# Performance work log

Hardware: AMD Instinct MI355X
Metric: run time of the kernel (lower is better)

## Reference

```python
import jax, jax.numpy as jnp
import numpy as np

B, S, D_MODEL, H = 4, 2048, 1024, 16
D_K = D_MODEL // H


def setup_inputs() -> dict:
    key = jax.random.key(0)
    kx, kq, kk, kv, ko = jax.random.split(key, 5)
    scale = 1.0 / np.sqrt(D_MODEL)
    return {
        "x": jax.random.normal(kx, (B, S, D_MODEL), dtype=jnp.float32),
        "W_q": jax.random.normal(kq, (D_MODEL, D_MODEL), dtype=jnp.float32) * scale,
        "W_k": jax.random.normal(kk, (D_MODEL, D_MODEL), dtype=jnp.float32) * scale,
        "W_v": jax.random.normal(kv, (D_MODEL, D_MODEL), dtype=jnp.float32) * scale,
        "W_out": jax.random.normal(ko, (D_MODEL, D_MODEL), dtype=jnp.float32) * scale,
    }


def reference(x, W_q, W_k, W_v, W_out):
    # nn.Linear(bias=False): y = x @ W.T; weights stored as (out, in).
    Bx, Sx, D = x.shape
    q = (x @ W_q.T).reshape(Bx, Sx, H, D_K).transpose(0, 2, 1, 3)  # (B,H,S,d_k)
    k = (x @ W_k.T).reshape(Bx, Sx, H, D_K).transpose(0, 2, 1, 3)
    v = (x @ W_v.T).reshape(Bx, Sx, H, D_K).transpose(0, 2, 1, 3)
    scores = jnp.einsum("bhsd,bhtd->bhst", q, k) / jnp.sqrt(jnp.float32(D_K))
    attn = jax.nn.softmax(scores, axis=-1)
    out = jnp.einsum("bhst,bhtd->bhsd", attn, v)  # (B,H,S,d_k)
    out = out.transpose(0, 2, 1, 3).reshape(Bx, Sx, D)  # combine heads
    return out @ W_out.T
```

## Files before the change

### kernel.cpp

```cpp
#include <hip/hip_runtime.h>

#define BATCH 4
#define SEQ 2048
#define DM 1024
#define NH 16
#define DK 64

typedef unsigned short u16;
typedef unsigned int u32;
typedef __attribute__((ext_vector_type(8))) short bfrag;
typedef __attribute__((ext_vector_type(4))) short bfrag4;
typedef __attribute__((ext_vector_type(4))) float ffrag;

__device__ inline u16 f2bf(float f) {
  union { float f; u32 u; } v; v.f = f;
  u32 u = v.u;
  return (u16)((u + 0x7FFFu + ((u >> 16) & 1u)) >> 16);
}
__device__ inline float bf2f(u16 u) {
  union { u32 u; float f; } v; v.u = ((u32)u) << 16;
  return v.f;
}
__device__ inline ffrag MFMA(bfrag a, bfrag b, ffrag c) {
  return __builtin_amdgcn_mfma_f32_16x16x32_bf16(a, b, c, 0, 0, 0);
}
#if defined(__has_builtin)
#if __has_builtin(__builtin_amdgcn_mfma_f32_16x16x16bf16_1k)
#define HAVE_MFMA16 1
#endif
#endif
#if HAVE_MFMA16
__device__ inline ffrag MFMA16(bfrag4 a, bfrag4 b, ffrag c) {
  return __builtin_amdgcn_mfma_f32_16x16x16bf16_1k(a, b, c, 0, 0, 0);
}
#else
__device__ inline ffrag MFMA16(bfrag4 a, bfrag4 b, ffrag c) { return c; }
#endif

__device__ __forceinline__ void g2l16(const u16* g, u16* l) {
  __builtin_amdgcn_global_load_lds(
      (const __attribute__((address_space(1))) u16*)g,
      (__attribute__((address_space(3))) u16*)l, 16, 0, 0);
}

__global__ __launch_bounds__(256) void cvt_all(
    const float* __restrict__ x,
    const float* __restrict__ a, const float* __restrict__ b,
    const float* __restrict__ c, const float* __restrict__ d,
    u16* __restrict__ ox,
    u16* __restrict__ oa, u16* __restrict__ ob,
    u16* __restrict__ oc, u16* __restrict__ od) {
  int blk = blockIdx.x;
  const float* in;
  u16* out;
  int i;
  if (blk < 8192) {
    in = x; out = ox; i = blk * 256 + threadIdx.x;
  } else {
    int wb = blk - 8192;
    int which = wb >> 10;
    in = which == 0 ? a : which == 1 ? b : which == 2 ? c : d;
    out = which == 0 ? oa : which == 1 ? ob : which == 2 ? oc : od;
    i = (wb & 1023) * 256 + threadIdx.x;
  }
  float4 v = ((const float4*)in)[i];
  union { u16 u[4]; uint2 dd; } o;
  o.u[0] = f2bf(v.x); o.u[1] = f2bf(v.y); o.u[2] = f2bf(v.z); o.u[3] = f2bf(v.w);
  ((uint2*)out)[i] = o.dd;
}

__global__ __launch_bounds__(256) void gemm_qkv(
    const u16* __restrict__ xb,
    const u16* __restrict__ Wq, const u16* __restrict__ Wk,
    const u16* __restrict__ Wv,
    u16* __restrict__ Qb, u16* __restrict__ Ksw, u16* __restrict__ Vsw) {
  const int z = blockIdx.z;
  const u16* Bm = z == 0 ? Wq : z == 1 ? Wk : Wv;

  const int K = DM;
  const int bm = blockIdx.y * 128, bn = blockIdx.x * 128;
  __shared__ __align__(16) u16 As[128 * 32];
  __shared__ __align__(16) u16 Bs[128 * 32];
  const int tid = threadIdx.x;
  const int lane = tid & 63;
  const int w = tid >> 6;
  const int wr = w >> 1, wc = w & 1;
  const int l15 = lane & 15, quad = lane >> 4;
  const int srow = tid >> 2, scol = (tid & 3) * 8;

  ffrag acc[4][4] = {};

  for (int k0 = 0; k0 < K; k0 += 32) {
    __syncthreads();
    g2l16(&xb[(size_t)(bm + srow) * K + k0 + scol], &As[tid * 8]);
    g2l16(&xb[(size_t)(bm + 64 + srow) * K + k0 + scol], &As[(tid + 256) * 8]);
    g2l16(&Bm[(size_t)(bn + srow) * K + k0 + scol], &Bs[tid * 8]);
    g2l16(&Bm[(size_t)(bn + 64 + srow) * K + k0 + scol], &Bs[(tid + 256) * 8]);
    __syncthreads();
    bfrag af[4], bf[4];
    if (z < 2) {
#pragma unroll
      for (int i = 0; i < 4; i++)
        af[i] = *(const bfrag*)(&As[(wr * 64 + i * 16 + l15) * 32 + quad * 8]);
#pragma unroll
      for (int j = 0; j < 4; j++)
        bf[j] = *(const bfrag*)(&Bs[(wc * 64 + j * 16 + l15) * 32 + quad * 8]);
    } else {
#pragma unroll
      for (int i = 0; i < 4; i++)
        af[i] = *(const bfrag*)(&Bs[(wr * 64 + i * 16 + l15) * 32 + quad * 8]);
#pragma unroll
      for (int j = 0; j < 4; j++)
        bf[j] = *(const bfrag*)(&As[(wc * 64 + j * 16 + l15) * 32 + quad * 8]);
    }
#pragma unroll
    for (int i = 0; i < 4; i++)
#pragma unroll
      for (int j = 0; j < 4; j++)
        acc[i][j] = MFMA(af[i], bf[j], acc[i][j]);
  }

  if (z == 0) {
#pragma unroll
    for (int i = 0; i < 4; i++)
#pragma unroll
      for (int j = 0; j < 4; j++)
#pragma unroll
        for (int r = 0; r < 4; r++) {
          int m = bm + wr * 64 + i * 16 + quad * 4 + r;
          int n = bn + wc * 64 + j * 16 + l15;
          int b = m >> 11, s = m & 2047;
          int h = n >> 6, d = n & 63;
          Qb[(((size_t)(b * NH + h)) * SEQ + s) * DK + d] = f2bf(acc[i][j][r]);
        }
  } else if (z == 1) {
#pragma unroll
    for (int i = 0; i < 4; i++)
#pragma unroll
      for (int j = 0; j < 4; j++)
#pragma unroll
        for (int r = 0; r < 4; r++) {
          int m = bm + wr * 64 + i * 16 + quad * 4 + r;
          int n = bn + wc * 64 + j * 16 + l15;
          int b = m >> 11, s = m & 2047;
          int h = n >> 6, d = n & 63;
          size_t hb = (size_t)(b * NH + h) * (SEQ * DK);
          size_t off = hb + (size_t)(s >> 6) * 4096 +
              ((((s >> 4) & 3) * 2 + (d >> 5)) * 64 +
               ((d >> 3) & 3) * 16 + (s & 15)) * 8 + (d & 7);
          Ksw[off] = f2bf(acc[i][j][r]);
        }
  } else {
#pragma unroll
    for (int i = 0; i < 4; i++)
#pragma unroll
      for (int j = 0; j < 4; j++)
#pragma unroll
        for (int r = 0; r < 4; r++) {
          int n = bn + wr * 64 + i * 16 + quad * 4 + r;
          int m = bm + wc * 64 + j * 16 + l15;
          int b = m >> 11, s = m & 2047;
          int h = n >> 6, d = n & 63;
          size_t hb = (size_t)(b * NH + h) * (SEQ * DK);
          size_t off = hb + (size_t)(s >> 6) * 4096 +
              ((((d >> 4) * 4 + ((s >> 4) & 3)) * 64 +
                ((s >> 2) & 3) * 16 + (d & 15)) * 4 + (s & 3));
          Vsw[off] = f2bf(acc[i][j][r]);
        }
  }
}

__global__ __launch_bounds__(256) void gemm_out(
    const u16* __restrict__ Ab, const u16* __restrict__ Wo, float* __restrict__ C) {
  const int K = DM, N = DM;
  const int bm = blockIdx.y * 128, bn = blockIdx.x * 128;
  __shared__ __align__(16) u16 As[128 * 32];
  __shared__ __align__(16) u16 Bs[128 * 32];
  const int tid = threadIdx.x;
  const int lane = tid & 63;
  const int w = tid >> 6;
  const int wr = w >> 1, wc = w & 1;
  const int l15 = lane & 15, quad = lane >> 4;
  const int srow = tid >> 2, scol = (tid & 3) * 8;

  ffrag acc[4][4] = {};

  for (int k0 = 0; k0 < K; k0 += 32) {
    __syncthreads();
    g2l16(&Ab[(size_t)(bm + srow) * K + k0 + scol], &As[tid * 8]);
    g2l16(&Ab[(size_t)(bm + 64 + srow) * K + k0 + scol], &As[(tid + 256) * 8]);
    g2l16(&Wo[(size_t)(bn + srow) * K + k0 + scol], &Bs[tid * 8]);
    g2l16(&Wo[(size_t)(bn + 64 + srow) * K + k0 + scol], &Bs[(tid + 256) * 8]);
    __syncthreads();
    bfrag af[4], bf[4];
#pragma unroll
    for (int i = 0; i < 4; i++)
      af[i] = *(const bfrag*)(&As[(wr * 64 + i * 16 + l15) * 32 + quad * 8]);
#pragma unroll
    for (int j = 0; j < 4; j++)
      bf[j] = *(const bfrag*)(&Bs[(wc * 64 + j * 16 + l15) * 32 + quad * 8]);
#pragma unroll
    for (int i = 0; i < 4; i++)
#pragma unroll
      for (int j = 0; j < 4; j++)
        acc[i][j] = MFMA(af[i], bf[j], acc[i][j]);
  }

#pragma unroll
  for (int i = 0; i < 4; i++)
#pragma unroll
    for (int j = 0; j < 4; j++)
#pragma unroll
      for (int r = 0; r < 4; r++) {
        int m = bm + wr * 64 + i * 16 + quad * 4 + r;
        int n = bn + wc * 64 + j * 16 + l15;
        C[(size_t)m * N + n] = acc[i][j][r];
      }
}

__global__ __launch_bounds__(256) void attn(
    const u16* __restrict__ Qb, const u16* __restrict__ Ksw,
    const u16* __restrict__ Vsw, u16* __restrict__ Ab) {
  const int bh = blockIdx.y;
  const int b = bh >> 4, h = bh & 15;
  const int qbase = blockIdx.x * 128;
  const int tid = threadIdx.x;
  const int w = tid >> 6, lane = tid & 63;
  const int l15 = lane & 15, quad = lane >> 4;

  __shared__ __align__(16) u16 Kt[2][4096];
  __shared__ __align__(16) u16 Vt[2][4096];

  const size_t hbase = (size_t)bh * SEQ * DK;

  const float qscale = 0.125f * 1.4426950408889634f;
  bfrag q[2][2];
#pragma unroll
  for (int i = 0; i < 2; i++)
#pragma unroll
    for (int kk = 0; kk < 2; kk++) {
      bfrag t = *(const bfrag*)(&Qb[hbase +
          (size_t)(qbase + w * 32 + i * 16 + l15) * DK + kk * 32 + quad * 8]);
#pragma unroll
      for (int e = 0; e < 8; e++)
        q[i][kk][e] = (short)f2bf(bf2f((u16)t[e]) * qscale);
    }

  ffrag O[4][2] = {};
  float lsum[2] = {0.f, 0.f};

  {
    const u16* ks = &Ksw[hbase];
    const u16* vs = &Vsw[hbase];
    g2l16(&ks[tid * 8], &Kt[0][tid * 8]);
    g2l16(&ks[2048 + tid * 8], &Kt[0][2048 + tid * 8]);
    g2l16(&vs[tid * 8], &Vt[0][tid * 8]);
    g2l16(&vs[2048 + tid * 8], &Vt[0][2048 + tid * 8]);
  }

  for (int t = 0; t < SEQ / 64; t++) {
    const int buf = t & 1;
    __syncthreads();
    if (t + 1 < SEQ / 64) {
      const u16* ks = &Ksw[hbase + (size_t)(t + 1) * 4096];
      const u16* vs = &Vsw[hbase + (size_t)(t + 1) * 4096];
      g2l16(&ks[tid * 8], &Kt[buf ^ 1][tid * 8]);
      g2l16(&ks[2048 + tid * 8], &Kt[buf ^ 1][2048 + tid * 8]);
      g2l16(&vs[tid * 8], &Vt[buf ^ 1][tid * 8]);
      g2l16(&vs[2048 + tid * 8], &Vt[buf ^ 1][2048 + tid * 8]);
    }

    __builtin_amdgcn_s_setprio(1);
    bfrag4 pb[4][2];
#pragma unroll
    for (int j = 0; j < 4; j++) {
      bfrag k0f = *(const bfrag*)(&Kt[buf][((j * 2 + 0) * 64 + lane) * 8]);
      bfrag k1f = *(const bfrag*)(&Kt[buf][((j * 2 + 1) * 64 + lane) * 8]);
#pragma unroll
      for (int i = 0; i < 2; i++) {
        ffrag z = {};
        z = MFMA(k0f, q[i][0], z);
        z = MFMA(k1f, q[i][1], z);
        u32 u[4]; float ts = 0.f;
#pragma unroll
        for (int r = 0; r < 4; r++) {
          float p = __builtin_amdgcn_exp2f(z[r]);
          u[r] = __float_as_uint(p);
          ts += __uint_as_float(u[r] & 0xffff0000u);
        }
        lsum[i] += ts;
        union { u32 d[2]; bfrag4 v; } pk;
        pk.d[0] = (u[1] & 0xffff0000u) | (u[0] >> 16);
        pk.d[1] = (u[3] & 0xffff0000u) | (u[2] >> 16);
        pb[j][i] = pk.v;
      }
    }

#pragma unroll
    for (int j = 0; j < 4; j++)
#pragma unroll
      for (int db = 0; db < 4; db++) {
        bfrag4 vf = *(const bfrag4*)(&Vt[buf][((db * 4 + j) * 64 + lane) * 4]);
        O[db][0] = MFMA16(vf, pb[j][0], O[db][0]);
        O[db][1] = MFMA16(vf, pb[j][1], O[db][1]);
      }
    __builtin_amdgcn_s_setprio(0);
  }

  float rl[2];
#pragma unroll
  for (int i = 0; i < 2; i++) {
    float s = lsum[i];
    s += __shfl_xor(s, 16);
    s += __shfl_xor(s, 32);
    rl[i] = 1.0f / s;
  }

  const size_t obase = ((size_t)b * SEQ) * DM + (size_t)h * DK;
#pragma unroll
  for (int db = 0; db < 4; db++)
#pragma unroll
    for (int i = 0; i < 2; i++) {
      int s = qbase + w * 32 + i * 16 + l15;
      union { u16 u[4]; uint2 d; } o;
#pragma unroll
      for (int r = 0; r < 4; r++) o.u[r] = f2bf(O[db][i][r] * rl[i]);
      *(uint2*)(&Ab[obase + (size_t)s * DM + db * 16 + quad * 4]) = o.d;
    }
}

extern "C" void kernel_launch(void* const* d_in, const int* in_sizes, int n_in,
                              void* d_out, int out_size, void* d_ws, size_t ws_size,
                              hipStream_t stream) {
  const float* x  = (const float*)d_in[0];
  const float* Wq = (const float*)d_in[1];
  const float* Wk = (const float*)d_in[2];
  const float* Wv = (const float*)d_in[3];
  const float* Wo = (const float*)d_in[4];
  float* out = (float*)d_out;

  char* ws = (char*)d_ws;
  u16* xb  = (u16*)(ws + 0);
  u16* Wqb = (u16*)(ws + 16777216);
  u16* Wkb = (u16*)(ws + 18874368);
  u16* Wvb = (u16*)(ws + 20971520);
  u16* Wob = (u16*)(ws + 23068672);
  u16* Qb  = (u16*)(ws + 25165824);
  u16* Ksw = (u16*)(ws + 41943040);
  u16* Vsw = (u16*)(ws + 58720256);
  u16* Ab  = (u16*)(ws + 75497472);
  const size_t NEED = 92274688;
  if (ws_size < NEED) return;

  cvt_all<<<12288, 256, 0, stream>>>(x, Wq, Wk, Wv, Wo, xb, Wqb, Wkb, Wvb, Wob);

  dim3 gqkv(DM / 128, (BATCH * SEQ) / 128, 3);
  gemm_qkv<<<gqkv, 256, 0, stream>>>(xb, Wqb, Wkb, Wvb, Qb, Ksw, Vsw);

  dim3 gat(SEQ / 128, BATCH * NH);
  attn<<<gat, 256, 0, stream>>>(Qb, Ksw, Vsw, Ab);

  dim3 gout(DM / 128, (BATCH * SEQ) / 128);
  gemm_out<<<gout, 256, 0, stream>>>(Ab, Wob, out);
}
```

Baseline: 292.4 us.

## Widen GEMM K-tile with XOR-swizzled LDS, sum softmax via MFMA, reorder attn grid

Both projection GEMMs now stage a K-depth of 64 per iteration instead of 32, halving the number of barrier pairs, and store tiles in LDS with an XOR swizzle on 16-byte chunks to avoid bank conflicts. In attention, the per-lane scalar row-sum plus cross-lane shuffles is replaced by an extra MFMA against a vector of ones that accumulates the softmax denominator. The attention grid is transposed so consecutive blocks cover different heads for the same query tile. The trade-off is twice the LDS per GEMM block, which may reduce occupancy, and one extra MFMA per P tile in the attention loop.

Measured after the change: 298.8 us. 1.02x slower.

```diff
diff --git a/kernel.cpp b/kernel.cpp
--- a/kernel.cpp
+++ b/kernel.cpp
@@ -79,45 +79,54 @@
 
   const int K = DM;
   const int bm = blockIdx.y * 128, bn = blockIdx.x * 128;
-  __shared__ __align__(16) u16 As[128 * 32];
-  __shared__ __align__(16) u16 Bs[128 * 32];
+  __shared__ __align__(16) u16 As[128 * 64];
+  __shared__ __align__(16) u16 Bs[128 * 64];
   const int tid = threadIdx.x;
   const int lane = tid & 63;
   const int w = tid >> 6;
   const int wr = w >> 1, wc = w & 1;
   const int l15 = lane & 15, quad = lane >> 4;
-  const int srow = tid >> 2, scol = (tid & 3) * 8;
+  const int srow = tid >> 3;
+  const int scol = (((tid & 7) ^ (srow & 7)) * 8);
 
   ffrag acc[4][4] = {};
 
-  for (int k0 = 0; k0 < K; k0 += 32) {
-    __syncthreads();
-    g2l16(&xb[(size_t)(bm + srow) * K + k0 + scol], &As[tid * 8]);
-    g2l16(&xb[(size_t)(bm + 64 + srow) * K + k0 + scol], &As[(tid + 256) * 8]);
-    g2l16(&Bm[(size_t)(bn + srow) * K + k0 + scol], &Bs[tid * 8]);
-    g2l16(&Bm[(size_t)(bn + 64 + srow) * K + k0 + scol], &Bs[(tid + 256) * 8]);
-    __syncthreads();
-    bfrag af[4], bf[4];
-    if (z < 2) {
+  for (int k0 = 0; k0 < K; k0 += 64) {
+    __syncthreads();
+#pragma unroll
+    for (int c = 0; c < 4; c++) {
+      g2l16(&xb[(size_t)(bm + c * 32 + srow) * K + k0 + scol], &As[c * 2048 + tid * 8]);
+      g2l16(&Bm[(size_t)(bn + c * 32 + srow) * K + k0 + scol], &Bs[c * 2048 + tid * 8]);
+    }
+    __syncthreads();
+#pragma unroll
+    for (int kk = 0; kk < 2; kk++) {
+      bfrag af[4], bf[4];
+      if (z < 2) {
+#pragma unroll
+        for (int i = 0; i < 4; i++)
+          af[i] = *(const bfrag*)(&As[(wr * 64 + i * 16 + l15) * 64 +
+                                      ((kk * 4 + quad) ^ (l15 & 7)) * 8]);
+#pragma unroll
+        for (int j = 0; j < 4; j++)
+          bf[j] = *(const bfrag*)(&Bs[(wc * 64 + j * 16 + l15) * 64 +
+                                      ((kk * 4 + quad) ^ (l15 & 7)) * 8]);
+      } else {
+#pragma unroll
+        for (int i = 0; i < 4; i++)
+          af[i] = *(const bfrag*)(&Bs[(wr * 64 + i * 16 + l15) * 64 +
+                                      ((kk * 4 + quad) ^ (l15 & 7)) * 8]);
+#pragma unroll
+        for (int j = 0; j < 4; j++)
+          bf[j] = *(const bfrag*)(&As[(wc * 64 + j * 16 + l15) * 64 +
+                                      ((kk * 4 + quad) ^ (l15 & 7)) * 8]);
+      }
 #pragma unroll
       for (int i = 0; i < 4; i++)
-        af[i] = *(const bfrag*)(&As[(wr * 64 + i * 16 + l15) * 32 + quad * 8]);
-#pragma unroll
-      for (int j = 0; j < 4; j++)
-        bf[j] = *(const bfrag*)(&Bs[(wc * 64 + j * 16 + l15) * 32 + quad * 8]);
-    } else {
-#pragma unroll
-      for (int i = 0; i < 4; i++)
-        af[i] = *(const bfrag*)(&Bs[(wr * 64 + i * 16 + l15) * 32 + quad * 8]);
-#pragma unroll
-      for (int j = 0; j < 4; j++)
-        bf[j] = *(const bfrag*)(&As[(wc * 64 + j * 16 + l15) * 32 + quad * 8]);
-    }
-#pragma unroll
-    for (int i = 0; i < 4; i++)
-#pragma unroll
-      for (int j = 0; j < 4; j++)
-        acc[i][j] = MFMA(af[i], bf[j], acc[i][j]);
+#pragma unroll
+        for (int j = 0; j < 4; j++)
+          acc[i][j] = MFMA(af[i], bf[j], acc[i][j]);
+    }
   }
 
   if (z == 0) {
@@ -174,36 +183,43 @@
     const u16* __restrict__ Ab, const u16* __restrict__ Wo, float* __restrict__ C) {
   const int K = DM, N = DM;
   const int bm = blockIdx.y * 128, bn = blockIdx.x * 128;
-  __shared__ __align__(16) u16 As[128 * 32];
-  __shared__ __align__(16) u16 Bs[128 * 32];
+  __shared__ __align__(16) u16 As[128 * 64];
+  __shared__ __align__(16) u16 Bs[128 * 64];
   const int tid = threadIdx.x;
   const int lane = tid & 63;
   const int w = tid >> 6;
   const int wr = w >> 1, wc = w & 1;
   const int l15 = lane & 15, quad = lane >> 4;
-  const int srow = tid >> 2, scol = (tid & 3) * 8;
+  const int srow = tid >> 3;
+  const int scol = (((tid & 7) ^ (srow & 7)) * 8);
 
   ffrag acc[4][4] = {};
 
-  for (int k0 = 0; k0 < K; k0 += 32) {
-    __syncthreads();
-    g2l16(&Ab[(size_t)(bm + srow) * K + k0 + scol], &As[tid * 8]);
-    g2l16(&Ab[(size_t)(bm + 64 + srow) * K + k0 + scol], &As[(tid + 256) * 8]);
-    g2l16(&Wo[(size_t)(bn + srow) * K + k0 + scol], &Bs[tid * 8]);
-    g2l16(&Wo[(size_t)(bn + 64 + srow) * K + k0 + scol], &Bs[(tid + 256) * 8]);
-    __syncthreads();
-    bfrag af[4], bf[4];
-#pragma unroll
-    for (int i = 0; i < 4; i++)
-      af[i] = *(const bfrag*)(&As[(wr * 64 + i * 16 + l15) * 32 + quad * 8]);
-#pragma unroll
-    for (int j = 0; j < 4; j++)
-      bf[j] = *(const bfrag*)(&Bs[(wc * 64 + j * 16 + l15) * 32 + quad * 8]);
-#pragma unroll
-    for (int i = 0; i < 4; i++)
+  for (int k0 = 0; k0 < K; k0 += 64) {
+    __syncthreads();
+#pragma unroll
+    for (int c = 0; c < 4; c++) {
+      g2l16(&Ab[(size_t)(bm + c * 32 + srow) * K + k0 + scol], &As[c * 2048 + tid * 8]);
+      g2l16(&Wo[(size_t)(bn + c * 32 + srow) * K + k0 + scol], &Bs[c * 2048 + tid * 8]);
+    }
+    __syncthreads();
+#pragma unroll
+    for (int kk = 0; kk < 2; kk++) {
+      bfrag af[4], bf[4];
+#pragma unroll
+      for (int i = 0; i < 4; i++)
+        af[i] = *(const bfrag*)(&As[(wr * 64 + i * 16 + l15) * 64 +
+                                    ((kk * 4 + quad) ^ (l15 & 7)) * 8]);
 #pragma unroll
       for (int j = 0; j < 4; j++)
-        acc[i][j] = MFMA(af[i], bf[j], acc[i][j]);
+        bf[j] = *(const bfrag*)(&Bs[(wc * 64 + j * 16 + l15) * 64 +
+                                    ((kk * 4 + quad) ^ (l15 & 7)) * 8]);
+#pragma unroll
+      for (int i = 0; i < 4; i++)
+#pragma unroll
+        for (int j = 0; j < 4; j++)
+          acc[i][j] = MFMA(af[i], bf[j], acc[i][j]);
+    }
   }
 
 #pragma unroll
@@ -221,9 +237,9 @@
 __global__ __launch_bounds__(256) void attn(
     const u16* __restrict__ Qb, const u16* __restrict__ Ksw,
     const u16* __restrict__ Vsw, u16* __restrict__ Ab) {
-  const int bh = blockIdx.y;
+  const int bh = blockIdx.x;
   const int b = bh >> 4, h = bh & 15;
-  const int qbase = blockIdx.x * 128;
+  const int qbase = blockIdx.y * 128;
   const int tid = threadIdx.x;
   const int w = tid >> 6, lane = tid & 63;
   const int l15 = lane & 15, quad = lane >> 4;
@@ -246,8 +262,10 @@
         q[i][kk][e] = (short)f2bf(bf2f((u16)t[e]) * qscale);
     }
 
+  const bfrag4 ones = {(short)0x3F80, (short)0x3F80, (short)0x3F80, (short)0x3F80};
+
   ffrag O[4][2] = {};
-  float lsum[2] = {0.f, 0.f};
+  ffrag Ls[2] = {};
 
   {
     const u16* ks = &Ksw[hbase];
@@ -281,18 +299,15 @@
         ffrag z = {};
         z = MFMA(k0f, q[i][0], z);
         z = MFMA(k1f, q[i][1], z);
-        u32 u[4]; float ts = 0.f;
-#pragma unroll
-        for (int r = 0; r < 4; r++) {
-          float p = __builtin_amdgcn_exp2f(z[r]);
-          u[r] = __float_as_uint(p);
-          ts += __uint_as_float(u[r] & 0xffff0000u);
-        }
-        lsum[i] += ts;
+        u32 u0 = __float_as_uint(__builtin_amdgcn_exp2f(z[0]));
+        u32 u1 = __float_as_uint(__builtin_amdgcn_exp2f(z[1]));
+        u32 u2 = __float_as_uint(__builtin_amdgcn_exp2f(z[2]));
+        u32 u3 = __float_as_uint(__builtin_amdgcn_exp2f(z[3]));
         union { u32 d[2]; bfrag4 v; } pk;
-        pk.d[0] = (u[1] & 0xffff0000u) | (u[0] >> 16);
-        pk.d[1] = (u[3] & 0xffff0000u) | (u[2] >> 16);
+        pk.d[0] = (u1 & 0xffff0000u) | (u0 >> 16);
+        pk.d[1] = (u3 & 0xffff0000u) | (u2 >> 16);
         pb[j][i] = pk.v;
+        Ls[i] = MFMA16(ones, pb[j][i], Ls[i]);
       }
     }
 
@@ -307,14 +322,7 @@
     __builtin_amdgcn_s_setprio(0);
   }
 
-  float rl[2];
-#pragma unroll
-  for (int i = 0; i < 2; i++) {
-    float s = lsum[i];
-    s += __shfl_xor(s, 16);
-    s += __shfl_xor(s, 32);
-    rl[i] = 1.0f / s;
-  }
+  const float rl[2] = {1.0f / Ls[0][0], 1.0f / Ls[1][0]};
 
   const size_t obase = ((size_t)b * SEQ) * DM + (size_t)h * DK;
 #pragma unroll
@@ -357,7 +365,7 @@
   dim3 gqkv(DM / 128, (BATCH * SEQ) / 128, 3);
   gemm_qkv<<<gqkv, 256, 0, stream>>>(xb, Wqb, Wkb, Wvb, Qb, Ksw, Vsw);
 
-  dim3 gat(SEQ / 128, BATCH * NH);
+  dim3 gat(BATCH * NH, SEQ / 128);
   attn<<<gat, 256, 0, stream>>>(Qb, Ksw, Vsw, Ab);
 
   dim3 gout(DM / 128, (BATCH * SEQ) / 128);
```
